# Performance work log

Hardware: AMD Instinct MI355X
Metric: run time of the kernel (lower is better)

The kernel has to match this reference:

```python
import jax, jax.numpy as jnp
import numpy as np

B, N = 32, 512
IN, HID, HEADS, OUT = 128, 32, 4, 128
NEG_SLOPE = 0.2


def _ln(x, g, b, eps=1e-5):
    mu = x.mean(-1, keepdims=True)
    var = ((x - mu) ** 2).mean(-1, keepdims=True)
    return (x - mu) * jax.lax.rsqrt(var + eps) * g + b


def _gat(x, adj_mask, W, a_src, a_dst, average):
    # x: [B,N,F], adj_mask: [B,1,N,N] bool, W: [F,H,D], a_*: [H,D]
    h = jnp.einsum('bnf,fhd->bnhd', x, W)                      # [B,N,H,D]
    e_src = jnp.einsum('bnhd,hd->bhn', h, a_src)               # [B,H,N]
    e_dst = jnp.einsum('bnhd,hd->bhn', h, a_dst)
    e = jax.nn.leaky_relu(e_src[:, :, :, None] + e_dst[:, :, None, :], NEG_SLOPE)  # [B,H,N,N]
    e = jnp.where(adj_mask, e, jnp.asarray(-1e9, e.dtype))
    att = jax.nn.softmax(e, axis=-1)                           # masked softmax over neighbors
    out = jnp.einsum('bhnm,bmhd->bnhd', att, h)                # aggregate neighbor features
    if average:
        return out.mean(axis=2)                                # [B,N,D]
    return out.reshape(out.shape[0], out.shape[1], -1)         # concat heads [B,N,H*D]


def setup_inputs() -> dict:
    key = jax.random.key(0)
    ks = jax.random.split(key, 16)
    def nrm(k, shape, scale=0.05):
        return jax.random.normal(k, shape, dtype=jnp.float32) * scale
    return {
        'x': jax.random.normal(ks[0], (B, N, IN), dtype=jnp.float32),
        'graph': jax.random.randint(ks[1], (B, N, N), 0, 2, dtype=jnp.int32),
        'W0': nrm(ks[2], (IN, HEADS, HID)),
        'a_src0': nrm(ks[3], (HEADS, HID)),
        'a_dst0': nrm(ks[4], (HEADS, HID)),
        'W1': nrm(ks[5], (HEADS * HID, 1, OUT)),
        'a_src1': nrm(ks[6], (1, OUT)),
        'a_dst1': nrm(ks[7], (1, OUT)),
        'ln1_g': jnp.ones((IN + OUT,), jnp.float32), 'ln1_b': jnp.zeros((IN + OUT,), jnp.float32),
        'lin_W': nrm(ks[8], (IN + OUT, OUT)), 'lin_b': jnp.zeros((OUT,), jnp.float32),
        'me_W0': nrm(ks[9], (OUT, OUT)), 'me_b0': jnp.zeros((OUT,), jnp.float32),
        'me_W1': nrm(ks[10], (OUT, OUT)), 'me_b1': jnp.zeros((OUT,), jnp.float32),
        'ln2_g': jnp.ones((OUT,), jnp.float32), 'ln2_b': jnp.zeros((OUT,), jnp.float32),
        'oh_W': nrm(ks[11], (OUT, OUT)), 'oh_b': jnp.zeros((OUT,), jnp.float32),
        'ln3_g': jnp.ones((OUT,), jnp.float32), 'ln3_b': jnp.zeros((OUT,), jnp.float32),
    }


def reference(x, graph, W0, a_src0, a_dst0, W1, a_src1, a_dst1,
              ln1_g, ln1_b, lin_W, lin_b, me_W0, me_b0, me_W1, me_b1,
              ln2_g, ln2_b, oh_W, oh_b, ln3_g, ln3_b):
    eye = jnp.eye(N, dtype=bool)
    adj_mask = ((graph > 0) | eye)[:, None, :, :]              # self-loops, [B,1,N,N]
    m = _gat(x, adj_mask, W0, a_src0, a_dst0, average=False)   # [B,N,HEADS*HID]
    m = jax.nn.elu(m)
    m = _gat(m, adj_mask, W1, a_src1, a_dst1, average=True)    # [B,N,OUT]
    m = _ln(jnp.concatenate([x, m], axis=-1), ln1_g, ln1_b)    # ln1
    m = m @ lin_W + lin_b                                      # linear
    enc = jax.nn.gelu(m @ me_W0 + me_b0, approximate=False) @ me_W1 + me_b1
    out = _ln(m + enc, ln2_g, ln2_b)                           # ln2(residual)
    out = jax.nn.gelu(out @ oh_W + oh_b, approximate=False)
    out = _ln(out, ln3_g, ln3_b)                               # LN inside output_head
    return out
```

## Files before the change

kernel.cpp:

```cpp
#include <hip/hip_runtime.h>
#include <cmath>


typedef unsigned short ushort_t;
typedef __attribute__((ext_vector_type(8))) short short8;
typedef __attribute__((ext_vector_type(4))) short s16x4;
typedef __attribute__((ext_vector_type(4))) float f32x4;

__device__ __forceinline__ float gelu_f(float v) {
    return 0.5f * v * (1.0f + erff(v * 0.70710678118654752f));
}
__device__ __forceinline__ ushort_t f2bf(float x) {
    union { float f; unsigned u; } v; v.f = x;
    return (ushort_t)((v.u + 0x7FFFu + ((v.u >> 16) & 1u)) >> 16);
}
__device__ __forceinline__ ushort_t f2bf_t(float x) {
    union { float f; unsigned u; } v; v.f = x;
    return (ushort_t)(v.u >> 16);
}

__device__ __forceinline__ void gload_lds16(const ushort_t* g, ushort_t* l) {
    __builtin_amdgcn_global_load_lds((__attribute__((address_space(1))) void*)g,
                                     (__attribute__((address_space(3))) void*)l, 16, 0, 0);
}
__device__ __forceinline__ void stage_chunk(const ushort_t* src, ushort_t* dst,
                                            int wv, int lane) {
#pragma unroll
    for (int i = 0; i < 4; i++) {
        int rbase = wv * 32 + i * 8;
        gload_lds16(src + (rbase + (lane >> 3)) * 512 + (lane & 7) * 8,
                    dst + rbase * 64);
    }
}

__global__ __launch_bounds__(256) void prep_wt(const float* __restrict__ lin_W,
        const float* __restrict__ me_W0, const float* __restrict__ me_W1,
        const float* __restrict__ oh_W, const float* __restrict__ W0,
        const float* __restrict__ W1, ushort_t* __restrict__ WT) {
    int i = blockIdx.x * 256 + threadIdx.x;
    if (i < 32768)       { int c = i >> 8, k = i & 255;                   WT[i] = f2bf(lin_W[k * 128 + c]); }
    else if (i < 49152)  { int j = i - 32768;  int c = j >> 7, k = j & 127; WT[i] = f2bf(me_W0[k * 128 + c]); }
    else if (i < 65536)  { int j = i - 49152;  int c = j >> 7, k = j & 127; WT[i] = f2bf(me_W1[k * 128 + c]); }
    else if (i < 81920)  { int j = i - 65536;  int c = j >> 7, k = j & 127; WT[i] = f2bf(oh_W[k * 128 + c]); }
    else if (i < 98304)  { int j = i - 81920;  int c = j >> 7, k = j & 127; WT[i] = f2bf(W0[k * 128 + c]); }
    else if (i < 114688) { int j = i - 98304;  int c = j >> 7, k = j & 127; WT[i] = f2bf(W1[k * 128 + c]); }
}

__global__ __launch_bounds__(256) void pack_graph(const int* __restrict__ g,
                                                  unsigned* __restrict__ gm) {
    int idx = blockIdx.x * 256 + threadIdx.x;
    const int4* gp = (const int4*)g + (size_t)idx * 8;
    unsigned m = 0;
#pragma unroll
    for (int q = 0; q < 8; q++) {
        int4 v = gp[q];
        m |= (unsigned)(v.x > 0) << (q * 4 + 0);
        m |= (unsigned)(v.y > 0) << (q * 4 + 1);
        m |= (unsigned)(v.z > 0) << (q * 4 + 2);
        m |= (unsigned)(v.w > 0) << (q * 4 + 3);
    }
    gm[idx] = m;
}

__global__ __launch_bounds__(256) void gemm_mfma0(const float* __restrict__ X,
        const ushort_t* __restrict__ WTr, ushort_t* __restrict__ Ht,
        const float* __restrict__ a_s, const float* __restrict__ a_d,
        float* __restrict__ es, float* __restrict__ ed) {
    __shared__ __align__(16) ushort_t abuf[16 * 128];
    __shared__ __align__(16) ushort_t tb[128 * 24];
    __shared__ float2 ered[8 * 16];
    const int tid = threadIdx.x;
    const int row0 = blockIdx.x * 16;
    const int b = row0 >> 9, m0 = row0 & 511;
    const int w = tid >> 6, lane = tid & 63;
    const int quad = lane >> 4, lid = lane & 15;
    {
        int r = tid >> 4, g = tid & 15;
        const float4* src = (const float4*)(X + (row0 + r) * 128 + g * 8);
        float4 a = src[0], bb = src[1];
        short8 p;
        p[0] = (short)f2bf(a.x);  p[1] = (short)f2bf(a.y);
        p[2] = (short)f2bf(a.z);  p[3] = (short)f2bf(a.w);
        p[4] = (short)f2bf(bb.x); p[5] = (short)f2bf(bb.y);
        p[6] = (short)f2bf(bb.z); p[7] = (short)f2bf(bb.w);
        *(short8*)&abuf[r * 128 + ((g ^ (r & 7)) * 8)] = p;
    }
    __syncthreads();
    short8 af[4];
#pragma unroll
    for (int kc = 0; kc < 4; kc++)
        af[kc] = *(const short8*)&abuf[lid * 128 + (((kc * 4 + quad) ^ (lid & 7)) * 8)];
    f32x4 C[2];
#pragma unroll
    for (int i = 0; i < 2; i++) {
        int ct = w + 4 * i;
        const ushort_t* bp = WTr + (ct * 16 + lid) * 128 + quad * 8;
        C[i] = (f32x4){0.f, 0.f, 0.f, 0.f};
#pragma unroll
        for (int kc = 0; kc < 4; kc++) {
            short8 bf = *(const short8*)&bp[kc * 32];
            C[i] = __builtin_amdgcn_mfma_f32_16x16x32_bf16(af[kc], bf, C[i], 0, 0, 0);
        }
    }
#pragma unroll
    for (int i = 0; i < 2; i++) {
        int ct = w + 4 * i, col = ct * 16 + lid;
        float as_c = a_s[col], ad_c = a_d[col];
        float s0[4], d0[4];
#pragma unroll
        for (int r = 0; r < 4; r++) { s0[r] = C[i][r] * as_c; d0[r] = C[i][r] * ad_c; }
#pragma unroll
        for (int st = 1; st <= 8; st <<= 1)
#pragma unroll
            for (int r = 0; r < 4; r++) {
                s0[r] += __shfl_xor(s0[r], st);
                d0[r] += __shfl_xor(d0[r], st);
            }
        if (lid == 0) {
#pragma unroll
            for (int r = 0; r < 4; r++)
                ered[ct * 16 + quad * 4 + r] = make_float2(s0[r], d0[r]);
        }
#pragma unroll
        for (int r = 0; r < 4; r++)
            tb[col * 24 + quad * 4 + r] = f2bf(C[i][r]);
    }
    __syncthreads();
    if (tid < 64) {
        int row = tid & 15, h = tid >> 4;
        float2 pa = ered[(2 * h) * 16 + row], pb = ered[(2 * h + 1) * 16 + row];
        es[(b * 4 + h) * 512 + m0 + row] = pa.x + pb.x;
        ed[(b * 4 + h) * 512 + m0 + row] = pa.y + pb.y;
    }
    {
        int c = tid >> 1, half = tid & 1;
        int m = m0 + half * 8;
        int msw = (m & ~63) | ((((m >> 3) ^ c) & 7) << 3);
        *(short8*)&Ht[b * 65536 + c * 512 + msw] = *(const short8*)&tb[c * 24 + half * 8];
    }
}

__global__ __launch_bounds__(256) void gat0_gemm(const ushort_t* __restrict__ Ht0,
        const float* __restrict__ es0, const float* __restrict__ ed0,
        const unsigned* __restrict__ gmask, const ushort_t* __restrict__ W1T,
        const float* __restrict__ a_s, const float* __restrict__ a_d,
        ushort_t* __restrict__ Ht1, float* __restrict__ es1, float* __restrict__ ed1) {
    __shared__ __align__(16) char smem[40960];
    ushort_t* hsb0 = (ushort_t*)smem;
    ushort_t* hsb1 = (ushort_t*)(smem + 16384);
    ushort_t* ps   = (ushort_t*)(smem + 32768);
    ushort_t* abuf = (ushort_t*)(smem + 32768);
    ushort_t* tb   = (ushort_t*)smem;
    float2*   ered = (float2*)(smem + 6144);
    const int tid = threadIdx.x;
    const int b = blockIdx.y, n0 = blockIdx.x * 16;
    const int wv = tid >> 6, lane = tid & 63;
    const int quad = lane >> 4, lid = lane & 15;
    const int pn = tid >> 4, pg = (tid >> 1) & 7, ph = tid & 1;
    const int ng = n0 + pn;
    const ushort_t* hsrc = Ht0 + b * 65536;
    const float es_r0 = es0[b * 2048 + (ph * 2) * 512 + ng];
    const float es_r1 = es0[b * 2048 + (ph * 2 + 1) * 512 + ng];
    const unsigned* gmrow = gmask + (b * 512 + ng) * 16;
    unsigned mword[8];
#pragma unroll
    for (int t = 0; t < 8; t++) mword[t] = gmrow[2 * t + (pg >> 2)];
    stage_chunk(hsrc, hsb0, wv, lane);
    const short8 onesf = {0x3F80, 0x3F80, 0x3F80, 0x3F80, 0x3F80, 0x3F80, 0x3F80, 0x3F80};
    f32x4 acc[2], dsf;
    acc[0] = (f32x4){0.f, 0.f, 0.f, 0.f};
    acc[1] = (f32x4){0.f, 0.f, 0.f, 0.f};
    dsf = (f32x4){0.f, 0.f, 0.f, 0.f};
#pragma unroll
    for (int t = 0; t < 8; t++) {
        const int mc = t * 64;
        ushort_t* cbuf = (t & 1) ? hsb1 : hsb0;
        const float* edg = ed0 + b * 2048 + mc + pg * 8;
        float4 eA0 = *(const float4*)&edg[(ph * 2) * 512];
        float4 eA1 = *(const float4*)&edg[(ph * 2) * 512 + 4];
        float4 eB0 = *(const float4*)&edg[(ph * 2 + 1) * 512];
        float4 eB1 = *(const float4*)&edg[(ph * 2 + 1) * 512 + 4];
        if (t < 7) stage_chunk(hsrc + mc + 64, (t & 1) ? hsb0 : hsb1, wv, lane);
        const int mbase = mc + pg * 8;
        unsigned mb8 = (mword[t] >> ((pg & 3) * 8)) & 0xffu;
        if ((unsigned)(ng - mbase) < 8u) mb8 |= 1u << (ng - mbase);
        {
            float ev[8] = {eA0.x, eA0.y, eA0.z, eA0.w, eA1.x, eA1.y, eA1.z, eA1.w};
            short8 pk;
#pragma unroll
            for (int j = 0; j < 8; j++) {
                float e = es_r0 + ev[j];
                e = fmaxf(e, 0.2f * e);
                e = ((mb8 >> j) & 1u) ? e : -1e30f;
                pk[j] = (short)f2bf_t(__expf(e));
            }
            int prow = (ph * 2) * 16 + pn;
            *(short8*)&ps[prow * 64 + ((pg ^ (prow & 7)) * 8)] = pk;
        }
        {
            float ev[8] = {eB0.x, eB0.y, eB0.z, eB0.w, eB1.x, eB1.y, eB1.z, eB1.w};
            short8 pk;
#pragma unroll
            for (int j = 0; j < 8; j++) {
                float e = es_r1 + ev[j];
                e = fmaxf(e, 0.2f * e);
                e = ((mb8 >> j) & 1u) ? e : -1e30f;
                pk[j] = (short)f2bf_t(__expf(e));
            }
            int prow = (ph * 2 + 1) * 16 + pn;
            *(short8*)&ps[prow * 64 + ((pg ^ (prow & 7)) * 8)] = pk;
        }
        if (t < 7) asm volatile("s_waitcnt vmcnt(4)" ::: "memory");
        else       asm volatile("s_waitcnt vmcnt(0)" ::: "memory");
        asm volatile("s_waitcnt lgkmcnt(0)" ::: "memory");
        __builtin_amdgcn_s_barrier();
        __builtin_amdgcn_sched_barrier(0);
#pragma unroll
        for (int kc = 0; kc < 2; kc++) {
            const int gsw = ((kc * 4 + quad) ^ (lid & 7)) * 8;
            short8 a = *(const short8*)&ps[(wv * 16 + lid) * 64 + gsw];
            short8 b0 = *(const short8*)&cbuf[(wv * 32 + lid) * 64 + gsw];
            short8 b1 = *(const short8*)&cbuf[(wv * 32 + 16 + lid) * 64 + gsw];
            acc[0] = __builtin_amdgcn_mfma_f32_16x16x32_bf16(a, b0, acc[0], 0, 0, 0);
            acc[1] = __builtin_amdgcn_mfma_f32_16x16x32_bf16(a, b1, acc[1], 0, 0, 0);
            dsf = __builtin_amdgcn_mfma_f32_16x16x32_bf16(a, onesf, dsf, 0, 0, 0);
        }
        __builtin_amdgcn_sched_barrier(0);
        __builtin_amdgcn_s_barrier();
        __builtin_amdgcn_sched_barrier(0);
    }
#pragma unroll
    for (int reg = 0; reg < 4; reg++) {
        float inv = 1.0f / dsf[reg];
        int rw = quad * 4 + reg;
#pragma unroll
        for (int ch = 0; ch < 2; ch++) {
            float v = acc[ch][reg] * inv;
            v = v > 0.f ? v : expm1f(v);
            int col = wv * 32 + ch * 16 + lid;
            abuf[rw * 128 + (((col >> 3) ^ (rw & 7)) * 8) + (col & 7)] = f2bf(v);
        }
    }
    __syncthreads();
    short8 af[4];
#pragma unroll
    for (int kc = 0; kc < 4; kc++)
        af[kc] = *(const short8*)&abuf[lid * 128 + (((kc * 4 + quad) ^ (lid & 7)) * 8)];
    f32x4 C[2];
#pragma unroll
    for (int i = 0; i < 2; i++) {
        int ct = wv + 4 * i;
        const ushort_t* bp = W1T + (ct * 16 + lid) * 128 + quad * 8;
        C[i] = (f32x4){0.f, 0.f, 0.f, 0.f};
#pragma unroll
        for (int kc = 0; kc < 4; kc++) {
            short8 bf = *(const short8*)&bp[kc * 32];
            C[i] = __builtin_amdgcn_mfma_f32_16x16x32_bf16(af[kc], bf, C[i], 0, 0, 0);
        }
    }
#pragma unroll
    for (int i = 0; i < 2; i++) {
        int ct = wv + 4 * i, col = ct * 16 + lid;
        float as_c = a_s[col], ad_c = a_d[col];
        float s0[4], d0[4];
#pragma unroll
        for (int r = 0; r < 4; r++) { s0[r] = C[i][r] * as_c; d0[r] = C[i][r] * ad_c; }
#pragma unroll
        for (int st = 1; st <= 8; st <<= 1)
#pragma unroll
            for (int r = 0; r < 4; r++) {
                s0[r] += __shfl_xor(s0[r], st);
                d0[r] += __shfl_xor(d0[r], st);
            }
        if (lid == 0) {
#pragma unroll
            for (int r = 0; r < 4; r++)
                ered[ct * 16 + quad * 4 + r] = make_float2(s0[r], d0[r]);
        }
#pragma unroll
        for (int r = 0; r < 4; r++)
            tb[col * 24 + quad * 4 + r] = f2bf(C[i][r]);
    }
    __syncthreads();
    if (tid < 16) {
        float S = 0.f, D = 0.f;
#pragma unroll
        for (int ct = 0; ct < 8; ct++) { float2 p = ered[ct * 16 + tid]; S += p.x; D += p.y; }
        es1[b * 512 + n0 + tid] = S;
        ed1[b * 512 + n0 + tid] = D;
    }
    {
        int c = tid >> 1, half = tid & 1;
        int m = n0 + half * 8;
        int msw = (m & ~63) | ((((m >> 3) ^ c) & 7) << 3);
        *(short8*)&Ht1[b * 65536 + c * 512 + msw] = *(const short8*)&tb[c * 24 + half * 8];
    }
}

__global__ __launch_bounds__(256) void gat1_head(const ushort_t* __restrict__ Ht,
        const float* __restrict__ es1, const float* __restrict__ ed1,
        const unsigned* __restrict__ gmask, const float* __restrict__ x,
        const float* __restrict__ g1, const float* __restrict__ b1,
        const ushort_t* __restrict__ linT, const float* __restrict__ LB,
        const ushort_t* __restrict__ meT0, const float* __restrict__ B0,
        const ushort_t* __restrict__ meT1, const float* __restrict__ B1,
        const float* __restrict__ g2, const float* __restrict__ b2,
        const ushort_t* __restrict__ ohT, const float* __restrict__ ob,
        const float* __restrict__ g3, const float* __restrict__ b3,
        float* __restrict__ out) {
    __shared__ __align__(16) char smem[36864];
    ushort_t* hsb0 = (ushort_t*)smem;
    ushort_t* hsb1 = (ushort_t*)(smem + 16384);
    ushort_t* ps   = (ushort_t*)(smem + 32768);
    float*    eds  = (float*)(smem + 34816);
    ushort_t* ybuf = (ushort_t*)smem;
    ushort_t* abuf = (ushort_t*)(smem + 8192);
    ushort_t* tbuf = (ushort_t*)(smem + 12288);
    float*    gbuf = (float*)(smem + 16384);
    float2*   red  = (float2*)(smem + 24832);
    float2*   mvs  = (float2*)(smem + 25344);
    const int tid = threadIdx.x;
    const int b = blockIdx.y, n0 = blockIdx.x * 16;
    const int wv = tid >> 6, lane = tid & 63;
    const int quad = lane >> 4, lid = lane & 15;
    const int pn = tid >> 4, q = tid & 15, off = q * 4;
    const int ng = n0 + pn;
    const ushort_t* hsrc = Ht + b * 65536;
    const float es_v = es1[b * 512 + ng];
    const unsigned* gmrow = gmask + (b * 512 + ng) * 16;
    unsigned mword[8];
#pragma unroll
    for (int t = 0; t < 8; t++) mword[t] = gmrow[2 * t + (q >> 3)];
    float2 edv = ((const float2*)(ed1 + b * 512))[tid];
    stage_chunk(hsrc, hsb0, wv, lane);
    ((float2*)eds)[tid] = edv;
    asm volatile("s_waitcnt lgkmcnt(0)" ::: "memory");
    __builtin_amdgcn_s_barrier();
    __builtin_amdgcn_sched_barrier(0);
    const short8 onesf = {0x3F80, 0x3F80, 0x3F80, 0x3F80, 0x3F80, 0x3F80, 0x3F80, 0x3F80};
    f32x4 acc[2], dsf;
    acc[0] = (f32x4){0.f, 0.f, 0.f, 0.f};
    acc[1] = (f32x4){0.f, 0.f, 0.f, 0.f};
    dsf = (f32x4){0.f, 0.f, 0.f, 0.f};
#pragma unroll
    for (int t = 0; t < 8; t++) {
        const int mc = t * 64;
        ushort_t* cbuf = (t & 1) ? hsb1 : hsb0;
        const int mbase = mc + off;
        float4 ev4 = *(const float4*)&eds[mbase];
        if (t < 7) stage_chunk(hsrc + mc + 64, (t & 1) ? hsb0 : hsb1, wv, lane);
        unsigned mb4 = (mword[t] >> ((q & 7) * 4)) & 0xFu;
        if ((unsigned)(ng - mbase) < 4u) mb4 |= 1u << (ng - mbase);
        float ev[4] = {ev4.x, ev4.y, ev4.z, ev4.w};
        s16x4 pk;
#pragma unroll
        for (int j = 0; j < 4; j++) {
            float e = es_v + ev[j];
            e = fmaxf(e, 0.2f * e);
            e = ((mb4 >> j) & 1u) ? e : -1e30f;
            pk[j] = (short)f2bf_t(__expf(e));
        }
        *(s16x4*)&ps[pn * 64 + (((off >> 3) ^ (pn & 7)) * 8) + (off & 7)] = pk;
        if (t < 7) asm volatile("s_waitcnt vmcnt(4)" ::: "memory");
        else       asm volatile("s_waitcnt vmcnt(0)" ::: "memory");
        asm volatile("s_waitcnt lgkmcnt(0)" ::: "memory");
        __builtin_amdgcn_s_barrier();
        __builtin_amdgcn_sched_barrier(0);
#pragma unroll
        for (int kc = 0; kc < 2; kc++) {
            const int gsw = ((kc * 4 + quad) ^ (lid & 7)) * 8;
            short8 a = *(const short8*)&ps[lid * 64 + gsw];
            short8 b0 = *(const short8*)&cbuf[(wv * 32 + lid) * 64 + gsw];
            short8 b1 = *(const short8*)&cbuf[(wv * 32 + 16 + lid) * 64 + gsw];
            acc[0] = __builtin_amdgcn_mfma_f32_16x16x32_bf16(a, b0, acc[0], 0, 0, 0);
            acc[1] = __builtin_amdgcn_mfma_f32_16x16x32_bf16(a, b1, acc[1], 0, 0, 0);
            dsf = __builtin_amdgcn_mfma_f32_16x16x32_bf16(a, onesf, dsf, 0, 0, 0);
        }
        __builtin_amdgcn_sched_barrier(0);
        __builtin_amdgcn_s_barrier();
        __builtin_amdgcn_sched_barrier(0);
    }
#pragma unroll
    for (int reg = 0; reg < 4; reg++) {
        float inv = 1.0f / dsf[reg];
        int rw = quad * 4 + reg;
#pragma unroll
        for (int ch = 0; ch < 2; ch++)
            gbuf[rw * 132 + wv * 32 + ch * 16 + lid] = acc[ch][reg] * inv;
    }
    __syncthreads();
    const int r = tid >> 4, c16 = tid & 15;
    const float4* xp = (const float4*)(x + (b * 512 + n0 + r) * 128);
    float4 vv4[4];
    float s = 0.f, ss = 0.f;
#pragma unroll
    for (int i = 0; i < 4; i++) {
        int c4 = c16 * 4 + i;
        float4 v = (c4 < 32) ? xp[c4] : *(const float4*)&gbuf[r * 132 + (c4 - 32) * 4];
        vv4[i] = v;
        s += v.x + v.y + v.z + v.w;
        ss += v.x * v.x + v.y * v.y + v.z * v.z + v.w * v.w;
    }
#pragma unroll
    for (int st = 1; st <= 8; st <<= 1) { s += __shfl_xor(s, st); ss += __shfl_xor(ss, st); }
    if (c16 == 0) {
        float mu = s * (1.f / 256.f);
        float var = ss * (1.f / 256.f) - mu * mu;
        mvs[r] = make_float2(mu, rsqrtf(var + 1e-5f));
    }
    __syncthreads();
    {
        float mu = mvs[r].x, rstd = mvs[r].y;
#pragma unroll
        for (int half = 0; half < 2; half++) {
            int g = c16 * 2 + half, c0 = g * 8;
            float va[8] = {vv4[half * 2].x, vv4[half * 2].y, vv4[half * 2].z, vv4[half * 2].w,
                           vv4[half * 2 + 1].x, vv4[half * 2 + 1].y, vv4[half * 2 + 1].z, vv4[half * 2 + 1].w};
            short8 p;
#pragma unroll
            for (int e = 0; e < 8; e++)
                p[e] = (short)f2bf((va[e] - mu) * rstd * g1[c0 + e] + b1[c0 + e]);
            *(short8*)&ybuf[r * 256 + ((g ^ (r & 7)) * 8)] = p;
        }
    }
    __syncthreads();
    short8 af8[8];
#pragma unroll
    for (int ks = 0; ks < 8; ks++)
        af8[ks] = *(const short8*)&ybuf[lid * 256 + (((ks * 4 + quad) ^ (lid & 7)) * 8)];
    f32x4 M2[2];
#pragma unroll
    for (int i = 0; i < 2; i++) {
        int ct = wv + 4 * i;
        const ushort_t* bp = linT + (ct * 16 + lid) * 256 + quad * 8;
        M2[i] = (f32x4){0.f, 0.f, 0.f, 0.f};
#pragma unroll
        for (int ks = 0; ks < 8; ks++) {
            short8 bf = *(const short8*)&bp[ks * 32];
            M2[i] = __builtin_amdgcn_mfma_f32_16x16x32_bf16(af8[ks], bf, M2[i], 0, 0, 0);
        }
        float bias = LB[ct * 16 + lid];
#pragma unroll
        for (int reg = 0; reg < 4; reg++) M2[i][reg] += bias;
        int col = ct * 16 + lid, g = col >> 3, pos = col & 7;
#pragma unroll
        for (int reg = 0; reg < 4; reg++) {
            int rw = quad * 4 + reg;
            abuf[rw * 128 + ((g ^ (rw & 7)) * 8) + pos] = f2bf(M2[i][reg]);
        }
    }
    __syncthreads();
    short8 at[4];
#pragma unroll
    for (int kc = 0; kc < 4; kc++)
        at[kc] = *(const short8*)&abuf[lid * 128 + (((kc * 4 + quad) ^ (lid & 7)) * 8)];
#pragma unroll
    for (int i = 0; i < 2; i++) {
        int ct = wv + 4 * i;
        const ushort_t* bp = meT0 + (ct * 16 + lid) * 128 + quad * 8;
        f32x4 C = (f32x4){0.f, 0.f, 0.f, 0.f};
#pragma unroll
        for (int kc = 0; kc < 4; kc++) {
            short8 bf = *(const short8*)&bp[kc * 32];
            C = __builtin_amdgcn_mfma_f32_16x16x32_bf16(at[kc], bf, C, 0, 0, 0);
        }
        int col = ct * 16 + lid, g = col >> 3, pos = col & 7;
        float bias = B0[col];
#pragma unroll
        for (int reg = 0; reg < 4; reg++) {
            int rw = quad * 4 + reg;
            tbuf[rw * 128 + ((g ^ (rw & 7)) * 8) + pos] = f2bf(gelu_f(C[reg] + bias));
        }
    }
    __syncthreads();
#pragma unroll
    for (int kc = 0; kc < 4; kc++)
        at[kc] = *(const short8*)&tbuf[lid * 128 + (((kc * 4 + quad) ^ (lid & 7)) * 8)];
    f32x4 R[2];
    float sr[4] = {0.f, 0.f, 0.f, 0.f}, ssr[4] = {0.f, 0.f, 0.f, 0.f};
#pragma unroll
    for (int i = 0; i < 2; i++) {
        int ct = wv + 4 * i;
        const ushort_t* bp = meT1 + (ct * 16 + lid) * 128 + quad * 8;
        f32x4 C = (f32x4){0.f, 0.f, 0.f, 0.f};
#pragma unroll
        for (int kc = 0; kc < 4; kc++) {
            short8 bf = *(const short8*)&bp[kc * 32];
            C = __builtin_amdgcn_mfma_f32_16x16x32_bf16(at[kc], bf, C, 0, 0, 0);
        }
        float bias = B1[ct * 16 + lid];
#pragma unroll
        for (int reg = 0; reg < 4; reg++) {
            float v = M2[i][reg] + C[reg] + bias;
            R[i][reg] = v;
            sr[reg] += v; ssr[reg] += v * v;
        }
    }
#pragma unroll
    for (int st = 1; st <= 8; st <<= 1)
#pragma unroll
        for (int reg = 0; reg < 4; reg++) {
            sr[reg] += __shfl_xor(sr[reg], st);
            ssr[reg] += __shfl_xor(ssr[reg], st);
        }
    if (lid == 0) {
#pragma unroll
        for (int reg = 0; reg < 4; reg++)
            red[wv * 16 + quad * 4 + reg] = make_float2(sr[reg], ssr[reg]);
    }
    __syncthreads();
    float mu2[4], rstd2[4];
#pragma unroll
    for (int reg = 0; reg < 4; reg++) {
        float S = 0.f, SS = 0.f;
#pragma unroll
        for (int w4 = 0; w4 < 4; w4++) {
            float2 p = red[w4 * 16 + quad * 4 + reg];
            S += p.x; SS += p.y;
        }
        mu2[reg] = S * (1.f / 128.f);
        float var = SS * (1.f / 128.f) - mu2[reg] * mu2[reg];
        rstd2[reg] = rsqrtf(var + 1e-5f);
    }
#pragma unroll
    for (int i = 0; i < 2; i++) {
        int col = (wv + 4 * i) * 16 + lid, g = col >> 3, pos = col & 7;
        float gv = g2[col], bv = b2[col];
#pragma unroll
        for (int reg = 0; reg < 4; reg++) {
            int rw = quad * 4 + reg;
            float v = (R[i][reg] - mu2[reg]) * rstd2[reg] * gv + bv;
            tbuf[rw * 128 + ((g ^ (rw & 7)) * 8) + pos] = f2bf(v);
        }
    }
    __syncthreads();
#pragma unroll
    for (int kc = 0; kc < 4; kc++)
        at[kc] = *(const short8*)&tbuf[lid * 128 + (((kc * 4 + quad) ^ (lid & 7)) * 8)];
    f32x4 V[2];
#pragma unroll
    for (int reg = 0; reg < 4; reg++) { sr[reg] = 0.f; ssr[reg] = 0.f; }
#pragma unroll
    for (int i = 0; i < 2; i++) {
        int ct = wv + 4 * i;
        const ushort_t* bp = ohT + (ct * 16 + lid) * 128 + quad * 8;
        f32x4 C = (f32x4){0.f, 0.f, 0.f, 0.f};
#pragma unroll
        for (int kc = 0; kc < 4; kc++) {
            short8 bf = *(const short8*)&bp[kc * 32];
            C = __builtin_amdgcn_mfma_f32_16x16x32_bf16(at[kc], bf, C, 0, 0, 0);
        }
        float bias = ob[ct * 16 + lid];
#pragma unroll
        for (int reg = 0; reg < 4; reg++) {
            float v = gelu_f(C[reg] + bias);
            V[i][reg] = v;
            sr[reg] += v; ssr[reg] += v * v;
        }
    }
#pragma unroll
    for (int st = 1; st <= 8; st <<= 1)
#pragma unroll
        for (int reg = 0; reg < 4; reg++) {
            sr[reg] += __shfl_xor(sr[reg], st);
            ssr[reg] += __shfl_xor(ssr[reg], st);
        }
    if (lid == 0) {
#pragma unroll
        for (int reg = 0; reg < 4; reg++)
            red[wv * 16 + quad * 4 + reg] = make_float2(sr[reg], ssr[reg]);
    }
    __syncthreads();
#pragma unroll
    for (int reg = 0; reg < 4; reg++) {
        float S = 0.f, SS = 0.f;
#pragma unroll
        for (int w4 = 0; w4 < 4; w4++) {
            float2 p = red[w4 * 16 + quad * 4 + reg];
            S += p.x; SS += p.y;
        }
        mu2[reg] = S * (1.f / 128.f);
        float var = SS * (1.f / 128.f) - mu2[reg] * mu2[reg];
        rstd2[reg] = rsqrtf(var + 1e-5f);
    }
#pragma unroll
    for (int i = 0; i < 2; i++) {
        int col = (wv + 4 * i) * 16 + lid;
        float gv = g3[col], bv = b3[col];
#pragma unroll
        for (int reg = 0; reg < 4; reg++)
            out[(b * 512 + n0 + quad * 4 + reg) * 128 + col] =
                (V[i][reg] - mu2[reg]) * rstd2[reg] * gv + bv;
    }
}

extern "C" void kernel_launch(void* const* d_in, const int* in_sizes, int n_in,
                              void* d_out, int out_size, void* d_ws, size_t ws_size,
                              hipStream_t stream) {
    const float* x      = (const float*)d_in[0];
    const int*   graph  = (const int*)d_in[1];
    const float* a_src0 = (const float*)d_in[3];
    const float* a_dst0 = (const float*)d_in[4];
    const float* a_src1 = (const float*)d_in[6];
    const float* a_dst1 = (const float*)d_in[7];
    float* out = (float*)d_out;

    float* ws  = (float*)d_ws;
    ushort_t* Ht0  = (ushort_t*)ws;
    ushort_t* Ht1  = Ht0 + 2097152;
    float*    e0s  = ws + 2097152;
    float*    e0d  = e0s + 65536;
    float*    e1s  = e0d + 65536;
    float*    e1d  = e1s + 16384;
    ushort_t* WT   = (ushort_t*)(e1d + 16384);
    ushort_t* linT = WT;
    ushort_t* meT0 = WT + 32768;
    ushort_t* meT1 = WT + 49152;
    ushort_t* ohT  = WT + 65536;
    ushort_t* W0T  = WT + 81920;
    ushort_t* W1T  = WT + 98304;
    unsigned* gmask = (unsigned*)(WT + 114688);

    prep_wt<<<448, 256, 0, stream>>>((const float*)d_in[10], (const float*)d_in[12],
                                     (const float*)d_in[14], (const float*)d_in[18],
                                     (const float*)d_in[2], (const float*)d_in[5], WT);
    pack_graph<<<1024, 256, 0, stream>>>(graph, gmask);
    gemm_mfma0<<<1024, 256, 0, stream>>>(x, W0T, Ht0, a_src0, a_dst0, e0s, e0d);
    gat0_gemm<<<dim3(32, 32), 256, 0, stream>>>(Ht0, e0s, e0d, gmask, W1T,
                                                a_src1, a_dst1, Ht1, e1s, e1d);
    gat1_head<<<dim3(32, 32), 256, 0, stream>>>(Ht1, e1s, e1d, gmask, x,
                                                (const float*)d_in[8], (const float*)d_in[9],
                                                linT, (const float*)d_in[11],
                                                meT0, (const float*)d_in[13],
                                                meT1, (const float*)d_in[15],
                                                (const float*)d_in[16], (const float*)d_in[17],
                                                ohT, (const float*)d_in[19],
                                                (const float*)d_in[20], (const float*)d_in[21],
                                                out);
}
```

Measured before the change: 185.9 us.

## Build attention probabilities directly in MFMA registers and drop per-chunk barriers

In both GAT aggregation kernels, each wave now computes its masked exp(leaky_relu) attention fragment straight into the MFMA A-operand layout. This replaces writing P to shared memory and reading it back. The per-chunk barriers and LDS waits are removed, the full mask row is loaded once as vectors, and in gat0 the ed row for the block's batch is staged into LDS once up front. In gat1 every wave now recomputes the same P tile, so exp work is duplicated. Correctness without barriers relies on each wave only reading the H rows it staged itself.

Measured after the change: 185.4 us. Within noise of the previous version (-0.3%).

```diff
diff --git a/kernel.cpp b/kernel.cpp
--- a/kernel.cpp
+++ b/kernel.cpp
@@ -4,7 +4,6 @@
 
 typedef unsigned short ushort_t;
 typedef __attribute__((ext_vector_type(8))) short short8;
-typedef __attribute__((ext_vector_type(4))) short s16x4;
 typedef __attribute__((ext_vector_type(4))) float f32x4;
 
 __device__ __forceinline__ float gelu_f(float v) {
@@ -148,7 +147,7 @@
     __shared__ __align__(16) char smem[40960];
     ushort_t* hsb0 = (ushort_t*)smem;
     ushort_t* hsb1 = (ushort_t*)(smem + 16384);
-    ushort_t* ps   = (ushort_t*)(smem + 32768);
+    float*    eds  = (float*)(smem + 32768);
     ushort_t* abuf = (ushort_t*)(smem + 32768);
     ushort_t* tb   = (ushort_t*)smem;
     float2*   ered = (float2*)(smem + 6144);
@@ -156,16 +155,28 @@
     const int b = blockIdx.y, n0 = blockIdx.x * 16;
     const int wv = tid >> 6, lane = tid & 63;
     const int quad = lane >> 4, lid = lane & 15;
-    const int pn = tid >> 4, pg = (tid >> 1) & 7, ph = tid & 1;
-    const int ng = n0 + pn;
+    const int n = n0 + lid;
     const ushort_t* hsrc = Ht0 + b * 65536;
-    const float es_r0 = es0[b * 2048 + (ph * 2) * 512 + ng];
-    const float es_r1 = es0[b * 2048 + (ph * 2 + 1) * 512 + ng];
-    const unsigned* gmrow = gmask + (b * 512 + ng) * 16;
-    unsigned mword[8];
-#pragma unroll
-    for (int t = 0; t < 8; t++) mword[t] = gmrow[2 * t + (pg >> 2)];
+    const float es_v = es0[b * 2048 + wv * 512 + n];
+    const unsigned* gmrow = gmask + (b * 512 + n) * 16;
+    uint4 gq0 = *(const uint4*)(gmrow);
+    uint4 gq1 = *(const uint4*)(gmrow + 4);
+    uint4 gq2 = *(const uint4*)(gmrow + 8);
+    uint4 gq3 = *(const uint4*)(gmrow + 12);
+    const unsigned mw[16] = {gq0.x, gq0.y, gq0.z, gq0.w, gq1.x, gq1.y, gq1.z, gq1.w,
+                             gq2.x, gq2.y, gq2.z, gq2.w, gq3.x, gq3.y, gq3.z, gq3.w};
+    {
+        const float4* src = (const float4*)(ed0 + b * 2048);
+        float4 v0 = src[tid * 2], v1 = src[tid * 2 + 1];
+        ((float4*)eds)[tid * 2] = v0;
+        ((float4*)eds)[tid * 2 + 1] = v1;
+    }
+    __builtin_amdgcn_sched_barrier(0);
     stage_chunk(hsrc, hsb0, wv, lane);
+    __builtin_amdgcn_sched_barrier(0);
+    asm volatile("s_waitcnt lgkmcnt(0)" ::: "memory");
+    __builtin_amdgcn_s_barrier();
+    __builtin_amdgcn_sched_barrier(0);
     const short8 onesf = {0x3F80, 0x3F80, 0x3F80, 0x3F80, 0x3F80, 0x3F80, 0x3F80, 0x3F80};
     f32x4 acc[2], dsf;
     acc[0] = (f32x4){0.f, 0.f, 0.f, 0.f};
@@ -173,62 +184,42 @@
     dsf = (f32x4){0.f, 0.f, 0.f, 0.f};
 #pragma unroll
     for (int t = 0; t < 8; t++) {
-        const int mc = t * 64;
         ushort_t* cbuf = (t & 1) ? hsb1 : hsb0;
-        const float* edg = ed0 + b * 2048 + mc + pg * 8;
-        float4 eA0 = *(const float4*)&edg[(ph * 2) * 512];
-        float4 eA1 = *(const float4*)&edg[(ph * 2) * 512 + 4];
-        float4 eB0 = *(const float4*)&edg[(ph * 2 + 1) * 512];
-        float4 eB1 = *(const float4*)&edg[(ph * 2 + 1) * 512 + 4];
-        if (t < 7) stage_chunk(hsrc + mc + 64, (t & 1) ? hsb0 : hsb1, wv, lane);
-        const int mbase = mc + pg * 8;
-        unsigned mb8 = (mword[t] >> ((pg & 3) * 8)) & 0xffu;
-        if ((unsigned)(ng - mbase) < 8u) mb8 |= 1u << (ng - mbase);
-        {
-            float ev[8] = {eA0.x, eA0.y, eA0.z, eA0.w, eA1.x, eA1.y, eA1.z, eA1.w};
+        short8 af[2];
+#pragma unroll
+        for (int kc = 0; kc < 2; kc++) {
+            const int base = t * 64 + kc * 32 + quad * 8;
+            unsigned mb8 = (mw[2 * t + kc] >> (quad * 8)) & 0xffu;
+            if ((unsigned)(n - base) < 8u) mb8 |= 1u << (n - base);
+            float4 e0v = *(const float4*)&eds[wv * 512 + base];
+            float4 e1v = *(const float4*)&eds[wv * 512 + base + 4];
+            float ev[8] = {e0v.x, e0v.y, e0v.z, e0v.w, e1v.x, e1v.y, e1v.z, e1v.w};
             short8 pk;
 #pragma unroll
             for (int j = 0; j < 8; j++) {
-                float e = es_r0 + ev[j];
+                float e = es_v + ev[j];
                 e = fmaxf(e, 0.2f * e);
                 e = ((mb8 >> j) & 1u) ? e : -1e30f;
                 pk[j] = (short)f2bf_t(__expf(e));
             }
-            int prow = (ph * 2) * 16 + pn;
-            *(short8*)&ps[prow * 64 + ((pg ^ (prow & 7)) * 8)] = pk;
-        }
-        {
-            float ev[8] = {eB0.x, eB0.y, eB0.z, eB0.w, eB1.x, eB1.y, eB1.z, eB1.w};
-            short8 pk;
-#pragma unroll
-            for (int j = 0; j < 8; j++) {
-                float e = es_r1 + ev[j];
-                e = fmaxf(e, 0.2f * e);
-                e = ((mb8 >> j) & 1u) ? e : -1e30f;
-                pk[j] = (short)f2bf_t(__expf(e));
-            }
-            int prow = (ph * 2 + 1) * 16 + pn;
-            *(short8*)&ps[prow * 64 + ((pg ^ (prow & 7)) * 8)] = pk;
-        }
+            af[kc] = pk;
+        }
+        if (t < 7) stage_chunk(hsrc + (t + 1) * 64, (t & 1) ? hsb0 : hsb1, wv, lane);
+        __builtin_amdgcn_sched_barrier(0);
         if (t < 7) asm volatile("s_waitcnt vmcnt(4)" ::: "memory");
         else       asm volatile("s_waitcnt vmcnt(0)" ::: "memory");
-        asm volatile("s_waitcnt lgkmcnt(0)" ::: "memory");
-        __builtin_amdgcn_s_barrier();
         __builtin_amdgcn_sched_barrier(0);
 #pragma unroll
         for (int kc = 0; kc < 2; kc++) {
             const int gsw = ((kc * 4 + quad) ^ (lid & 7)) * 8;
-            short8 a = *(const short8*)&ps[(wv * 16 + lid) * 64 + gsw];
             short8 b0 = *(const short8*)&cbuf[(wv * 32 + lid) * 64 + gsw];
             short8 b1 = *(const short8*)&cbuf[(wv * 32 + 16 + lid) * 64 + gsw];
-            acc[0] = __builtin_amdgcn_mfma_f32_16x16x32_bf16(a, b0, acc[0], 0, 0, 0);
-            acc[1] = __builtin_amdgcn_mfma_f32_16x16x32_bf16(a, b1, acc[1], 0, 0, 0);
-            dsf = __builtin_amdgcn_mfma_f32_16x16x32_bf16(a, onesf, dsf, 0, 0, 0);
-        }
-        __builtin_amdgcn_sched_barrier(0);
-        __builtin_amdgcn_s_barrier();
-        __builtin_amdgcn_sched_barrier(0);
-    }
+            acc[0] = __builtin_amdgcn_mfma_f32_16x16x32_bf16(af[kc], b0, acc[0], 0, 0, 0);
+            acc[1] = __builtin_amdgcn_mfma_f32_16x16x32_bf16(af[kc], b1, acc[1], 0, 0, 0);
+            dsf = __builtin_amdgcn_mfma_f32_16x16x32_bf16(af[kc], onesf, dsf, 0, 0, 0);
+        }
+    }
+    __syncthreads();
 #pragma unroll
     for (int reg = 0; reg < 4; reg++) {
         float inv = 1.0f / dsf[reg];
@@ -308,11 +299,10 @@
         const ushort_t* __restrict__ ohT, const float* __restrict__ ob,
         const float* __restrict__ g3, const float* __restrict__ b3,
         float* __restrict__ out) {
-    __shared__ __align__(16) char smem[36864];
+    __shared__ __align__(16) char smem[34816];
     ushort_t* hsb0 = (ushort_t*)smem;
     ushort_t* hsb1 = (ushort_t*)(smem + 16384);
-    ushort_t* ps   = (ushort_t*)(smem + 32768);
-    float*    eds  = (float*)(smem + 34816);
+    float*    eds  = (float*)(smem + 32768);
     ushort_t* ybuf = (ushort_t*)smem;
     ushort_t* abuf = (ushort_t*)(smem + 8192);
     ushort_t* tbuf = (ushort_t*)(smem + 12288);
@@ -323,17 +313,23 @@
     const int b = blockIdx.y, n0 = blockIdx.x * 16;
     const int wv = tid >> 6, lane = tid & 63;
     const int quad = lane >> 4, lid = lane & 15;
-    const int pn = tid >> 4, q = tid & 15, off = q * 4;
-    const int ng = n0 + pn;
+    const int n = n0 + lid;
     const ushort_t* hsrc = Ht + b * 65536;
-    const float es_v = es1[b * 512 + ng];
-    const unsigned* gmrow = gmask + (b * 512 + ng) * 16;
-    unsigned mword[8];
-#pragma unroll
-    for (int t = 0; t < 8; t++) mword[t] = gmrow[2 * t + (q >> 3)];
-    float2 edv = ((const float2*)(ed1 + b * 512))[tid];
+    const float es_v = es1[b * 512 + n];
+    const unsigned* gmrow = gmask + (b * 512 + n) * 16;
+    uint4 gq0 = *(const uint4*)(gmrow);
+    uint4 gq1 = *(const uint4*)(gmrow + 4);
+    uint4 gq2 = *(const uint4*)(gmrow + 8);
+    uint4 gq3 = *(const uint4*)(gmrow + 12);
+    const unsigned mw[16] = {gq0.x, gq0.y, gq0.z, gq0.w, gq1.x, gq1.y, gq1.z, gq1.w,
+                             gq2.x, gq2.y, gq2.z, gq2.w, gq3.x, gq3.y, gq3.z, gq3.w};
+    {
+        float2 edv = ((const float2*)(ed1 + b * 512))[tid];
+        ((float2*)eds)[tid] = edv;
+    }
+    __builtin_amdgcn_sched_barrier(0);
     stage_chunk(hsrc, hsb0, wv, lane);
-    ((float2*)eds)[tid] = edv;
+    __builtin_amdgcn_sched_barrier(0);
     asm volatile("s_waitcnt lgkmcnt(0)" ::: "memory");
     __builtin_amdgcn_s_barrier();
     __builtin_amdgcn_sched_barrier(0);
@@ -344,42 +340,42 @@
     dsf = (f32x4){0.f, 0.f, 0.f, 0.f};
 #pragma unroll
     for (int t = 0; t < 8; t++) {
-        const int mc = t * 64;
         ushort_t* cbuf = (t & 1) ? hsb1 : hsb0;
-        const int mbase = mc + off;
-        float4 ev4 = *(const float4*)&eds[mbase];
-        if (t < 7) stage_chunk(hsrc + mc + 64, (t & 1) ? hsb0 : hsb1, wv, lane);
-        unsigned mb4 = (mword[t] >> ((q & 7) * 4)) & 0xFu;
-        if ((unsigned)(ng - mbase) < 4u) mb4 |= 1u << (ng - mbase);
-        float ev[4] = {ev4.x, ev4.y, ev4.z, ev4.w};
-        s16x4 pk;
-#pragma unroll
-        for (int j = 0; j < 4; j++) {
-            float e = es_v + ev[j];
-            e = fmaxf(e, 0.2f * e);
-            e = ((mb4 >> j) & 1u) ? e : -1e30f;
-            pk[j] = (short)f2bf_t(__expf(e));
-        }
-        *(s16x4*)&ps[pn * 64 + (((off >> 3) ^ (pn & 7)) * 8) + (off & 7)] = pk;
+        short8 af[2];
+#pragma unroll
+        for (int kc = 0; kc < 2; kc++) {
+            const int base = t * 64 + kc * 32 + quad * 8;
+            unsigned mb8 = (mw[2 * t + kc] >> (quad * 8)) & 0xffu;
+            if ((unsigned)(n - base) < 8u) mb8 |= 1u << (n - base);
+            float4 e0v = *(const float4*)&eds[base];
+            float4 e1v = *(const float4*)&eds[base + 4];
+            float ev[8] = {e0v.x, e0v.y, e0v.z, e0v.w, e1v.x, e1v.y, e1v.z, e1v.w};
+            short8 pk;
+#pragma unroll
+            for (int j = 0; j < 8; j++) {
+                float e = es_v + ev[j];
+                e = fmaxf(e, 0.2f * e);
+                e = ((mb8 >> j) & 1u) ? e : -1e30f;
+                pk[j] = (short)f2bf_t(__expf(e));
+            }
+            af[kc] = pk;
+        }
+        if (t < 7) stage_chunk(hsrc + (t + 1) * 64, (t & 1) ? hsb0 : hsb1, wv, lane);
+        __builtin_amdgcn_sched_barrier(0);
         if (t < 7) asm volatile("s_waitcnt vmcnt(4)" ::: "memory");
         else       asm volatile("s_waitcnt vmcnt(0)" ::: "memory");
-        asm volatile("s_waitcnt lgkmcnt(0)" ::: "memory");
-        __builtin_amdgcn_s_barrier();
         __builtin_amdgcn_sched_barrier(0);
 #pragma unroll
         for (int kc = 0; kc < 2; kc++) {
             const int gsw = ((kc * 4 + quad) ^ (lid & 7)) * 8;
-            short8 a = *(const short8*)&ps[lid * 64 + gsw];
             short8 b0 = *(const short8*)&cbuf[(wv * 32 + lid) * 64 + gsw];
             short8 b1 = *(const short8*)&cbuf[(wv * 32 + 16 + lid) * 64 + gsw];
-            acc[0] = __builtin_amdgcn_mfma_f32_16x16x32_bf16(a, b0, acc[0], 0, 0, 0);
-            acc[1] = __builtin_amdgcn_mfma_f32_16x16x32_bf16(a, b1, acc[1], 0, 0, 0);
-            dsf = __builtin_amdgcn_mfma_f32_16x16x32_bf16(a, onesf, dsf, 0, 0, 0);
-        }
-        __builtin_amdgcn_sched_barrier(0);
-        __builtin_amdgcn_s_barrier();
-        __builtin_amdgcn_sched_barrier(0);
-    }
+            acc[0] = __builtin_amdgcn_mfma_f32_16x16x32_bf16(af[kc], b0, acc[0], 0, 0, 0);
+            acc[1] = __builtin_amdgcn_mfma_f32_16x16x32_bf16(af[kc], b1, acc[1], 0, 0, 0);
+            dsf = __builtin_amdgcn_mfma_f32_16x16x32_bf16(af[kc], onesf, dsf, 0, 0, 0);
+        }
+    }
+    __syncthreads();
 #pragma unroll
     for (int reg = 0; reg < 4; reg++) {
         float inv = 1.0f / dsf[reg];
```
